# Kernel optimization log

Hardware: AMD Instinct MI355X
Metric: run time of the kernel (lower is better)

Reference implementation:

```python
import jax, jax.numpy as jnp
import numpy as np

VOCAB = 29
VEC = 512      # vector_dim
HID = 1024     # hidden_size
SEN = 64       # sen_len (== seq length)
BATCH = 2048


def setup_inputs() -> dict:
    key = jax.random.key(0)
    k1, k2, k3, k4, k5, k6 = jax.random.split(key, 6)
    s_emb = 1.0
    s_ih = 1.0 / np.sqrt(HID)
    s_cls = 1.0 / np.sqrt(HID)
    return {
        "x": jax.random.randint(k1, (BATCH, SEN), 0, VOCAB, dtype=jnp.int64),
        "emb": jax.random.normal(k2, (VOCAB, VEC), dtype=jnp.float32) * s_emb,
        "W_ih": jax.random.uniform(k3, (HID, VEC), dtype=jnp.float32, minval=-s_ih, maxval=s_ih),
        "W_hh": jax.random.uniform(k4, (HID, HID), dtype=jnp.float32, minval=-s_ih, maxval=s_ih),
        "W_cls": jax.random.uniform(k5, (SEN + 1, HID), dtype=jnp.float32, minval=-s_cls, maxval=s_cls),
        "b_cls": jax.random.uniform(k6, (SEN + 1,), dtype=jnp.float32, minval=-s_cls, maxval=s_cls),
    }


def reference(x, emb, W_ih, W_hh, W_cls, b_cls):
    # Embedding lookup: [B, S, VEC]
    xe = emb[x]
    # Precompute input projections for all timesteps: [B, S, HID]
    xin = jnp.einsum("bsv,hv->bsh", xe, W_ih)

    def step(h, x_t):
        # h: [B, HID], x_t: [B, HID] (already W_ih @ x)
        h_new = jnp.tanh(x_t + h @ W_hh.T)
        return h_new, None

    h0 = jnp.zeros((x.shape[0], HID), dtype=xin.dtype)
    h_last, _ = jax.lax.scan(step, h0, jnp.swapaxes(xin, 0, 1))  # scan over S

    # h.squeeze() in torch (num_layers=1) -> [B, HID]
    logits = h_last @ W_cls.T + b_cls  # [B, SEN+1]
    return logits
```

## Files before the change

kernel.cpp:

```cpp
#include <hip/hip_runtime.h>
#include <hip/hip_bf16.h>

#define VOCAB 29
#define VEC   512
#define HID   1024
#define SEN   64
#define BATCH 2048

typedef __bf16 bf16_t;
typedef bf16_t bf16x8 __attribute__((ext_vector_type(8)));
typedef float  floatx4 __attribute__((ext_vector_type(4)));

__global__ void cvt_whh(const float* __restrict__ w, bf16_t* __restrict__ o, int n) {
    int i = blockIdx.x * blockDim.x + threadIdx.x;
    if (i < n) o[i] = (bf16_t)w[i];
}

__global__ void cvt_wcls(const float* __restrict__ w, bf16_t* __restrict__ o) {
    int i = blockIdx.x * blockDim.x + threadIdx.x;
    if (i >= 80 * HID) return;
    o[i] = (i < 65 * HID) ? (bf16_t)w[i] : (bf16_t)0.0f;
}

__global__ void proj_kernel(const float* __restrict__ emb, const float* __restrict__ wih,
                            float* __restrict__ proj) {
    int idx = blockIdx.x * blockDim.x + threadIdx.x;
    if (idx >= VOCAB * HID) return;
    int v = idx / HID, h = idx % HID;
    const float* e = emb + v * VEC;
    const float* w = wih + h * VEC;
    float s = 0.f;
    for (int k = 0; k < VEC; k += 4) {
        float4 ev = *(const float4*)(e + k);
        float4 wv = *(const float4*)(w + k);
        s += ev.x * wv.x + ev.y * wv.y + ev.z * wv.z + ev.w * wv.w;
    }
    proj[idx] = s;
}

__device__ __forceinline__ float fast_tanh(float x) {
    float e = __expf(2.0f * x);
    return 1.0f - 2.0f / (e + 1.0f);
}

__device__ __forceinline__ void load16_to_lds(const bf16_t* g, bf16_t* l) {
    auto gp = reinterpret_cast<const __attribute__((address_space(1))) unsigned int*>(
        reinterpret_cast<uintptr_t>(g));
    auto lp = reinterpret_cast<__attribute__((address_space(3))) unsigned int*>(
        static_cast<unsigned int>(reinterpret_cast<uintptr_t>(l)));
    __builtin_amdgcn_global_load_lds(gp, lp, 16, 0, 0);
}

#define BM 128
#define BN 64
#define BK 64

__global__ __launch_bounds__(256)
void rnn_step(const bf16_t* __restrict__ h_in, const bf16_t* __restrict__ whh,
              const float* __restrict__ proj, const int* __restrict__ x,
              bf16_t* __restrict__ h_out, int t, int first)
{
    __shared__ __align__(16) bf16_t Ash[2][BM][BK];
    __shared__ __align__(16) bf16_t Bsh[2][BN][BK];
    __shared__ int tok_sh[BM];

    const int tid  = threadIdx.x;
    const int m0   = blockIdx.x * BM;
    const int n0   = blockIdx.y * BN;
    const int wave = tid >> 6;
    const int lane = tid & 63;
    const int wm   = wave * 32;
    const int q    = lane >> 4;
    const int l16  = lane & 15;

    if (tid < BM) tok_sh[tid] = x[(m0 + tid) * SEN + t];

    const bf16_t* srcA[4];
    const bf16_t* srcB[2];
    int dstA[4], dstB[2];
#pragma unroll
    for (int it = 0; it < 4; it++) {
        int c = it * 256 + wave * 64 + lane;
        int r = c >> 3, p = c & 7, g = p ^ (r & 7);
        srcA[it] = h_in + (m0 + r) * HID + g * 8;
        dstA[it] = (it * 256 + wave * 64) * 8;
    }
#pragma unroll
    for (int it = 0; it < 2; it++) {
        int c = it * 256 + wave * 64 + lane;
        int r = c >> 3, p = c & 7, g = p ^ (r & 7);
        srcB[it] = whh + (n0 + r) * HID + g * 8;
        dstB[it] = (it * 256 + wave * 64) * 8;
    }

    floatx4 acc[2][4];
#pragma unroll
    for (int i = 0; i < 2; i++)
#pragma unroll
        for (int j = 0; j < 4; j++) acc[i][j] = (floatx4){0.f, 0.f, 0.f, 0.f};

    if (!first) {
#pragma unroll
        for (int it = 0; it < 4; it++) load16_to_lds(srcA[it], &Ash[0][0][0] + dstA[it]);
#pragma unroll
        for (int it = 0; it < 2; it++) load16_to_lds(srcB[it], &Bsh[0][0][0] + dstB[it]);
    }
    __syncthreads();

    if (!first) {
        for (int i = 0; i < 16; i++) {
            const int buf = i & 1;
            if (i < 15) {
                const int koff = (i + 1) * BK;
#pragma unroll
                for (int it = 0; it < 4; it++)
                    load16_to_lds(srcA[it] + koff, &Ash[1 - buf][0][0] + dstA[it]);
#pragma unroll
                for (int it = 0; it < 2; it++)
                    load16_to_lds(srcB[it] + koff, &Bsh[1 - buf][0][0] + dstB[it]);
            }
#pragma unroll
            for (int ks = 0; ks < BK; ks += 32) {
                const int pq = (((ks >> 3) + q) ^ (l16 & 7)) * 8;
                bf16x8 af[2], bfr[4];
                af[0]  = *(const bf16x8*)&Ash[buf][wm + l16][pq];
                af[1]  = *(const bf16x8*)&Ash[buf][wm + 16 + l16][pq];
                bfr[0] = *(const bf16x8*)&Bsh[buf][l16][pq];
                bfr[1] = *(const bf16x8*)&Bsh[buf][16 + l16][pq];
                bfr[2] = *(const bf16x8*)&Bsh[buf][32 + l16][pq];
                bfr[3] = *(const bf16x8*)&Bsh[buf][48 + l16][pq];
#pragma unroll
                for (int mi = 0; mi < 2; mi++)
#pragma unroll
                    for (int ni = 0; ni < 4; ni++)
                        acc[mi][ni] = __builtin_amdgcn_mfma_f32_16x16x32_bf16(
                            af[mi], bfr[ni], acc[mi][ni], 0, 0, 0);
            }
            if (i < 15) __syncthreads();
        }
    }

#pragma unroll
    for (int mi = 0; mi < 2; mi++) {
#pragma unroll
        for (int r = 0; r < 4; r++) {
            int lm = wm + mi * 16 + q * 4 + r;
            int gm = m0 + lm;
            const float* pr = proj + tok_sh[lm] * HID;
#pragma unroll
            for (int ni = 0; ni < 4; ni++) {
                int gn = n0 + ni * 16 + l16;
                float v = acc[mi][ni][r] + pr[gn];
                h_out[gm * HID + gn] = (bf16_t)fast_tanh(v);
            }
        }
    }
}

#define CBM 128
#define CLDK 72
__global__ __launch_bounds__(256)
void classifier_mfma(const bf16_t* __restrict__ h, const bf16_t* __restrict__ wcls,
                     const float* __restrict__ bcls, float* __restrict__ out)
{
    __shared__ __align__(16) bf16_t Ash[CBM][CLDK];
    __shared__ __align__(16) bf16_t Bsh[80][CLDK];

    const int tid = threadIdx.x;
    const int m0 = blockIdx.x * CBM;
    const int wave = tid >> 6, lane = tid & 63;
    const int wm = wave * 32;
    const int q = lane >> 4, l16 = lane & 15;

    floatx4 acc[2][5];
#pragma unroll
    for (int i = 0; i < 2; i++)
#pragma unroll
        for (int j = 0; j < 5; j++) acc[i][j] = (floatx4){0.f, 0.f, 0.f, 0.f};

    for (int kk = 0; kk < HID; kk += 64) {
#pragma unroll
        for (int it = 0; it < 4; it++) {
            int idx = tid + it * 256, r = idx >> 3, c = (idx & 7) * 8;
            *(uint4*)&Ash[r][c] = *(const uint4*)&h[(m0 + r) * HID + kk + c];
        }
#pragma unroll
        for (int it = 0; it < 3; it++) {
            int idx = tid + it * 256;
            if (idx < 640) {
                int r = idx >> 3, c = (idx & 7) * 8;
                *(uint4*)&Bsh[r][c] = *(const uint4*)&wcls[r * HID + kk + c];
            }
        }
        __syncthreads();
#pragma unroll
        for (int ks = 0; ks < 64; ks += 32) {
            bf16x8 af[2], bfr[5];
#pragma unroll
            for (int mi = 0; mi < 2; mi++)
                af[mi] = *(const bf16x8*)&Ash[wm + mi * 16 + l16][ks + q * 8];
#pragma unroll
            for (int ni = 0; ni < 5; ni++)
                bfr[ni] = *(const bf16x8*)&Bsh[ni * 16 + l16][ks + q * 8];
#pragma unroll
            for (int mi = 0; mi < 2; mi++)
#pragma unroll
                for (int ni = 0; ni < 5; ni++)
                    acc[mi][ni] = __builtin_amdgcn_mfma_f32_16x16x32_bf16(
                        af[mi], bfr[ni], acc[mi][ni], 0, 0, 0);
        }
        __syncthreads();
    }

#pragma unroll
    for (int mi = 0; mi < 2; mi++) {
#pragma unroll
        for (int r = 0; r < 4; r++) {
            int gm = m0 + wm + mi * 16 + q * 4 + r;
#pragma unroll
            for (int ni = 0; ni < 5; ni++) {
                int gn = ni * 16 + l16;
                if (gn < SEN + 1)
                    out[gm * (SEN + 1) + gn] = acc[mi][ni][r] + bcls[gn];
            }
        }
    }
}

extern "C" void kernel_launch(void* const* d_in, const int* in_sizes, int n_in,
                              void* d_out, int out_size, void* d_ws, size_t ws_size,
                              hipStream_t stream)
{
    const int*   x     = (const int*)  d_in[0];
    const float* emb   = (const float*)d_in[1];
    const float* w_ih  = (const float*)d_in[2];
    const float* w_hh  = (const float*)d_in[3];
    const float* w_cls = (const float*)d_in[4];
    const float* b_cls = (const float*)d_in[5];
    float* out = (float*)d_out;

    char* ws = (char*)d_ws;
    bf16_t* whh_bf  = (bf16_t*)ws;
    float*  proj    = (float*)(ws + (2u << 20));
    bf16_t* wcls_bf = (bf16_t*)(ws + (2u << 20) + (128u << 10));
    bf16_t* h0      = (bf16_t*)(ws + (2u << 20) + (288u << 10));
    bf16_t* h1      = (bf16_t*)(ws + (6u << 20) + (288u << 10));

    cvt_whh<<<(HID * HID) / 256, 256, 0, stream>>>(w_hh, whh_bf, HID * HID);
    proj_kernel<<<(VOCAB * HID + 255) / 256, 256, 0, stream>>>(emb, w_ih, proj);
    cvt_wcls<<<(80 * HID) / 256, 256, 0, stream>>>(w_cls, wcls_bf);

    dim3 grid(BATCH / BM, HID / BN);
    bf16_t* bufs[2] = {h0, h1};
    for (int t = 0; t < SEN; t++) {
        bf16_t* hi = bufs[(t + 1) & 1];
        bf16_t* ho = bufs[t & 1];
        rnn_step<<<grid, 256, 0, stream>>>(hi, whh_bf, proj, x, ho, t, t == 0 ? 1 : 0);
    }
    classifier_mfma<<<BATCH / CBM, 256, 0, stream>>>(bufs[1], wcls_bf, b_cls, out);
}
```

Measured before the change: 781.0 us.

## Stage full W_hh tile in LDS and stream h directly into registers

Replaces the double-buffered 64-wide K loop with a single LDS buffer holding the block's whole 64x1024 W_hh slice, loaded in two halves so compute on the first half overlaps the second load. Activation fragments for h are read straight from global memory into registers, with software prefetch across groups of eight K steps. This cuts the per-step barriers from sixteen to two and removes the LDS round trip for A. The trade-off is about 128KB of LDS per block, which limits occupancy to one block per CU, and A reads that are less coalesced.

```diff
diff --git a/kernel.cpp b/kernel.cpp
--- a/kernel.cpp
+++ b/kernel.cpp
@@ -53,15 +53,13 @@
 
 #define BM 128
 #define BN 64
-#define BK 64
 
 __global__ __launch_bounds__(256)
 void rnn_step(const bf16_t* __restrict__ h_in, const bf16_t* __restrict__ whh,
               const float* __restrict__ proj, const int* __restrict__ x,
               bf16_t* __restrict__ h_out, int t, int first)
 {
-    __shared__ __align__(16) bf16_t Ash[2][BM][BK];
-    __shared__ __align__(16) bf16_t Bsh[2][BN][BK];
+    __shared__ __align__(16) bf16_t Bsh[BN][HID];
     __shared__ int tok_sh[BM];
 
     const int tid  = threadIdx.x;
@@ -72,73 +70,75 @@
     const int wm   = wave * 32;
     const int q    = lane >> 4;
     const int l16  = lane & 15;
+    const int l7   = l16 & 7;
 
     if (tid < BM) tok_sh[tid] = x[(m0 + tid) * SEN + t];
 
-    const bf16_t* srcA[4];
-    const bf16_t* srcB[2];
-    int dstA[4], dstB[2];
-#pragma unroll
-    for (int it = 0; it < 4; it++) {
-        int c = it * 256 + wave * 64 + lane;
-        int r = c >> 3, p = c & 7, g = p ^ (r & 7);
-        srcA[it] = h_in + (m0 + r) * HID + g * 8;
-        dstA[it] = (it * 256 + wave * 64) * 8;
-    }
-#pragma unroll
-    for (int it = 0; it < 2; it++) {
-        int c = it * 256 + wave * 64 + lane;
-        int r = c >> 3, p = c & 7, g = p ^ (r & 7);
-        srcB[it] = whh + (n0 + r) * HID + g * 8;
-        dstB[it] = (it * 256 + wave * 64) * 8;
-    }
-
     floatx4 acc[2][4];
 #pragma unroll
     for (int i = 0; i < 2; i++)
 #pragma unroll
         for (int j = 0; j < 4; j++) acc[i][j] = (floatx4){0.f, 0.f, 0.f, 0.f};
 
+    const bf16_t* hA = h_in + (m0 + wm + l16) * HID + q * 8;
+
+    bf16x8 af[2][8][2];
+
+#define ISSUE_AF(BUF, KBASE)                                                     \
+    _Pragma("unroll")                                                            \
+    for (int j = 0; j < 8; j++) {                                                \
+        af[BUF][j][0] = *(const bf16x8*)(hA + ((KBASE) + j) * 32);               \
+        af[BUF][j][1] = *(const bf16x8*)(hA + 16 * HID + ((KBASE) + j) * 32);    \
+    }
+
+#define COMPUTE_GROUP(BUF, KBASE)                                                \
+    _Pragma("unroll")                                                            \
+    for (int j = 0; j < 8; j++) {                                                \
+        const int p = (4 * ((KBASE) + j) + q) ^ l7;   \
+        bf16x8 b0 = *(const bf16x8*)&Bsh[l16][p * 8];                            \
+        bf16x8 b1 = *(const bf16x8*)&Bsh[16 + l16][p * 8];                       \
+        bf16x8 b2 = *(const bf16x8*)&Bsh[32 + l16][p * 8];                       \
+        bf16x8 b3 = *(const bf16x8*)&Bsh[48 + l16][p * 8];                       \
+        acc[0][0] = __builtin_amdgcn_mfma_f32_16x16x32_bf16(af[BUF][j][0], b0, acc[0][0], 0, 0, 0); \
+        acc[0][1] = __builtin_amdgcn_mfma_f32_16x16x32_bf16(af[BUF][j][0], b1, acc[0][1], 0, 0, 0); \
+        acc[0][2] = __builtin_amdgcn_mfma_f32_16x16x32_bf16(af[BUF][j][0], b2, acc[0][2], 0, 0, 0); \
+        acc[0][3] = __builtin_amdgcn_mfma_f32_16x16x32_bf16(af[BUF][j][0], b3, acc[0][3], 0, 0, 0); \
+        acc[1][0] = __builtin_amdgcn_mfma_f32_16x16x32_bf16(af[BUF][j][1], b0, acc[1][0], 0, 0, 0); \
+        acc[1][1] = __builtin_amdgcn_mfma_f32_16x16x32_bf16(af[BUF][j][1], b1, acc[1][1], 0, 0, 0); \
+        acc[1][2] = __builtin_amdgcn_mfma_f32_16x16x32_bf16(af[BUF][j][1], b2, acc[1][2], 0, 0, 0); \
+        acc[1][3] = __builtin_amdgcn_mfma_f32_16x16x32_bf16(af[BUF][j][1], b3, acc[1][3], 0, 0, 0); \
+    }
+
     if (!first) {
 #pragma unroll
-        for (int it = 0; it < 4; it++) load16_to_lds(srcA[it], &Ash[0][0][0] + dstA[it]);
-#pragma unroll
-        for (int it = 0; it < 2; it++) load16_to_lds(srcB[it], &Bsh[0][0][0] + dstB[it]);
+        for (int it = 0; it < 16; it++) {
+            const int r = it * 4 + wave;
+            load16_to_lds(whh + (n0 + r) * HID + (lane ^ (r & 7)) * 8,
+                          &Bsh[r][lane * 8]);
+        }
+        ISSUE_AF(0, 0)
     }
     __syncthreads();
 
     if (!first) {
-        for (int i = 0; i < 16; i++) {
-            const int buf = i & 1;
-            if (i < 15) {
-                const int koff = (i + 1) * BK;
-#pragma unroll
-                for (int it = 0; it < 4; it++)
-                    load16_to_lds(srcA[it] + koff, &Ash[1 - buf][0][0] + dstA[it]);
-#pragma unroll
-                for (int it = 0; it < 2; it++)
-                    load16_to_lds(srcB[it] + koff, &Bsh[1 - buf][0][0] + dstB[it]);
-            }
-#pragma unroll
-            for (int ks = 0; ks < BK; ks += 32) {
-                const int pq = (((ks >> 3) + q) ^ (l16 & 7)) * 8;
-                bf16x8 af[2], bfr[4];
-                af[0]  = *(const bf16x8*)&Ash[buf][wm + l16][pq];
-                af[1]  = *(const bf16x8*)&Ash[buf][wm + 16 + l16][pq];
-                bfr[0] = *(const bf16x8*)&Bsh[buf][l16][pq];
-                bfr[1] = *(const bf16x8*)&Bsh[buf][16 + l16][pq];
-                bfr[2] = *(const bf16x8*)&Bsh[buf][32 + l16][pq];
-                bfr[3] = *(const bf16x8*)&Bsh[buf][48 + l16][pq];
-#pragma unroll
-                for (int mi = 0; mi < 2; mi++)
-#pragma unroll
-                    for (int ni = 0; ni < 4; ni++)
-                        acc[mi][ni] = __builtin_amdgcn_mfma_f32_16x16x32_bf16(
-                            af[mi], bfr[ni], acc[mi][ni], 0, 0, 0);
-            }
-            if (i < 15) __syncthreads();
-        }
-    }
+#pragma unroll
+        for (int it = 0; it < 16; it++) {
+            const int r = it * 4 + wave;
+            load16_to_lds(whh + (n0 + r) * HID + 512 + (lane ^ (r & 7)) * 8,
+                          &Bsh[r][512 + lane * 8]);
+        }
+        ISSUE_AF(1, 8)
+        COMPUTE_GROUP(0, 0)
+        ISSUE_AF(0, 16)
+        COMPUTE_GROUP(1, 8)
+        __syncthreads();
+        ISSUE_AF(1, 24)
+        COMPUTE_GROUP(0, 16)
+        COMPUTE_GROUP(1, 24)
+    }
+
+#undef ISSUE_AF
+#undef COMPUTE_GROUP
 
 #pragma unroll
     for (int mi = 0; mi < 2; mi++) {
```

Result: slower. 922.4 us (+18.1%).
